# Optimization experiments

Hardware: AMD Instinct MI355X
Metric: run time of the kernel (lower is better)

## Reference

```python
import jax, jax.numpy as jnp
import numpy as np

INPUT_SIZE = 128
HIDDEN_SIZE = 256
OUTPUT_SIZE = 64
BATCH = 128
SEQ_LEN = 2048


def _xavier(key, shape):
    fan_in, fan_out = shape[1], shape[0]
    std = (2.0 / (fan_in + fan_out)) ** 0.5
    return jax.random.normal(key, shape, dtype=jnp.float32) * std


def setup_inputs() -> dict:
    key = jax.random.key(0)
    ks = jax.random.split(key, 5)
    gru_in = INPUT_SIZE + OUTPUT_SIZE  # Jordan feedback: input concat prev output
    return {
        "x": jax.random.normal(ks[0], (BATCH, SEQ_LEN, INPUT_SIZE), dtype=jnp.float32),
        "w_ih": _xavier(ks[1], (3 * HIDDEN_SIZE, gru_in)),   # [r|z|n] input weights
        "w_hh": _xavier(ks[2], (3 * HIDDEN_SIZE, HIDDEN_SIZE)),
        "b_ih": jnp.zeros((3 * HIDDEN_SIZE,), dtype=jnp.float32),
        "b_hh": jnp.zeros((3 * HIDDEN_SIZE,), dtype=jnp.float32),
        "fc_w": _xavier(ks[3], (OUTPUT_SIZE, HIDDEN_SIZE)),
        "fc_b": jnp.zeros((OUTPUT_SIZE,), dtype=jnp.float32),
    }


def reference(x, w_ih, w_hh, b_ih, b_hh, fc_w, fc_b):
    B = x.shape[0]
    H = w_hh.shape[1]
    O = fc_w.shape[0]

    def step(carry, x_t):
        h, y_prev = carry  # h: [B,H], y_prev: [B,O]
        inp = jnp.concatenate([x_t, y_prev], axis=-1)       # [B, I+O]
        gi = inp @ w_ih.T + b_ih                            # [B, 3H]
        gh = h @ w_hh.T + b_hh                              # [B, 3H]
        i_r, i_z, i_n = jnp.split(gi, 3, axis=-1)
        h_r, h_z, h_n = jnp.split(gh, 3, axis=-1)
        r = jax.nn.sigmoid(i_r + h_r)
        z = jax.nn.sigmoid(i_z + h_z)
        n = jnp.tanh(i_n + r * h_n)
        h_new = (1.0 - z) * n + z * h                       # PyTorch GRU update
        y = jnp.tanh(h_new @ fc_w.T + fc_b)                 # Jordan output feedback
        return (h_new, y), None

    xs = jnp.swapaxes(x, 0, 1)  # [T, B, I] for scan over time
    h0 = jnp.zeros((B, H), dtype=x.dtype)
    y0 = jnp.zeros((B, O), dtype=x.dtype)
    (h_last, y_last), _ = jax.lax.scan(step, (h0, y0), xs)
    return y_last  # matches outputs[:, -1, :]
```

## Files before the change

kernel.cpp:

```cpp
#include <hip/hip_runtime.h>
#include <math.h>


#define TSTEPS 2048
#define ISZ 128

typedef _Float16 half8 __attribute__((ext_vector_type(8)));
typedef float f32x4 __attribute__((ext_vector_type(4)));
typedef unsigned int u32;
typedef unsigned int u32x4 __attribute__((ext_vector_type(4)));
typedef unsigned long long u64;

__device__ __forceinline__ f32x4 mfma16(half8 a, half8 b, f32x4 c) {
  return __builtin_amdgcn_mfma_f32_16x16x32_f16(a, b, c, 0, 0, 0);
}
__device__ __forceinline__ float sigm(float x) {
  return __builtin_amdgcn_rcpf(1.f + __expf(-x));
}
__device__ __forceinline__ float tanh_fast(float x) {
  return 1.f - 2.f * __builtin_amdgcn_rcpf(1.f + __expf(2.f * x));
}
__device__ __forceinline__ float asf(u32 u) {
  union { u32 v; float f; } c; c.v = u; return c.f;
}

__device__ __forceinline__ void st_pkt(void* p, u32x4 v) {
  asm volatile("global_store_dwordx4 %0, %1, off sc1" :: "v"(p), "v"(v) : "memory");
}
__device__ __forceinline__ void ld_pkt3_issue(const void* p1, const void* p2,
                                              const void* p3, u32x4& r1, u32x4& r2,
                                              u32x4& r3) {
  asm volatile("global_load_dwordx4 %0, %3, off sc1\n\t"
               "global_load_dwordx4 %1, %4, off sc1\n\t"
               "global_load_dwordx4 %2, %5, off sc1"
               : "=&v"(r1), "=&v"(r2), "=&v"(r3)
               : "v"(p1), "v"(p2), "v"(p3) : "memory");
}
__device__ __forceinline__ void ld_pkt3_wait(const void* p1, const void* p2,
                                             const void* p3, u32x4& r1, u32x4& r2,
                                             u32x4& r3) {
  asm volatile("global_load_dwordx4 %0, %3, off sc1\n\t"
               "global_load_dwordx4 %1, %4, off sc1\n\t"
               "global_load_dwordx4 %2, %5, off sc1\n\t"
               "s_waitcnt vmcnt(0)"
               : "=&v"(r1), "=&v"(r2), "=&v"(r3)
               : "v"(p1), "v"(p2), "v"(p3) : "memory");
}
__device__ __forceinline__ void ld_x2(const float* p, u32x4& x0, u32x4& x1) {
  asm volatile("global_load_dwordx4 %0, %2, off\n\t"
               "global_load_dwordx4 %1, %3, off"
               : "=&v"(x0), "=&v"(x1)
               : "v"(p), "v"(p + 4) : "memory");
}
#define PKT_OK(r, tgt) (((r)[2] >= (tgt)) && (((r)[0] ^ (r)[1] ^ (r)[2]) == (r)[3]))
#define SB() __builtin_amdgcn_sched_barrier(0)

__global__ __attribute__((amdgpu_flat_work_group_size(256, 256),
                          amdgpu_waves_per_eu(1, 1)))
void jordan_rnn(const float* __restrict__ xg, const float* __restrict__ w_ih,
                const float* __restrict__ w_hh, const float* __restrict__ b_ih,
                const float* __restrict__ b_hh, const float* __restrict__ fc_w,
                const float* __restrict__ fc_b, float* __restrict__ out,
                unsigned char* __restrict__ ws)
{
  const int tid  = threadIdx.x;
  const int lane = tid & 63;
  const int wv   = tid >> 6;
  const int n    = lane & 15;
  const int quad = lane >> 4;
  const int col  = blockIdx.x & 7;
  const int q    = blockIdx.x >> 3;
  const int u0   = q * 64 + wv * 16;
  const int b0   = col * 16;

  unsigned char* pay = ws;

  __shared__ _Float16 act[16][456];
  {
    unsigned int* za = (unsigned int*)&act[0][0];
    for (int i = tid; i < 3648; i += 256) za[i] = 0u;
  }

  half8 wr[14], wz[14], win[6], whn[8], wfc[8];
  {
    const int kq = quad * 8;
    const int ur = u0 + n, uz = 256 + u0 + n, un = 512 + u0 + n;
#pragma unroll
    for (int kk = 0; kk < 6; ++kk) {
      const float* pr = w_ih + ur * 192 + kk * 32 + kq;
      const float* pz = w_ih + uz * 192 + kk * 32 + kq;
      const float* pn = w_ih + un * 192 + kk * 32 + kq;
#pragma unroll
      for (int j = 0; j < 8; ++j) {
        wr[kk][j] = (_Float16)pr[j]; wz[kk][j] = (_Float16)pz[j]; win[kk][j] = (_Float16)pn[j];
      }
    }
#pragma unroll
    for (int kk = 0; kk < 8; ++kk) {
      const float* pr = w_hh + ur * 256 + kk * 32 + kq;
      const float* pz = w_hh + uz * 256 + kk * 32 + kq;
      const float* pn = w_hh + un * 256 + kk * 32 + kq;
#pragma unroll
      for (int j = 0; j < 8; ++j) {
        wr[6 + kk][j] = (_Float16)pr[j]; wz[6 + kk][j] = (_Float16)pz[j]; whn[kk][j] = (_Float16)pn[j];
      }
    }
#pragma unroll
    for (int kk = 0; kk < 8; ++kk) {
      const float* pf = fc_w + (wv * 16 + n) * 256 + kk * 32 + kq;
#pragma unroll
      for (int j = 0; j < 8; ++j) wfc[kk][j] = (_Float16)pf[j];
    }
  }
  const float br   = b_ih[u0 + n] + b_hh[u0 + n];
  const float bz   = b_ih[256 + u0 + n] + b_hh[256 + u0 + n];
  const float bin_ = b_ih[512 + u0 + n];
  const float bhn  = b_hh[512 + u0 + n];
  const float fcb  = fc_b[wv * 16 + n];

  float hprev[4] = {0.f, 0.f, 0.f, 0.f};

  const int xr = tid >> 4, xc = tid & 15;
  const int sblk = tid >> 6, srem = tid & 63;
  const int cr = (srem >> 4) * 4;
  const int cc = srem & 15;
  const int ok0 = 6 + 2 * q;
  const int fk0 = 2 * q;
  const int q1 = (q + 1) & 3, q2 = (q + 2) & 3, q3 = (q + 3) & 3;

  unsigned char* cb0 = pay + (size_t)col * 16384;
  unsigned char* cb1 = cb0 + 131072;
  const int poff = (q * 4 + wv) * 1024 + lane * 16;
  const int off1 = (q1 * 4 + sblk) * 1024 + srem * 16;
  const int off2 = (q2 * 4 + sblk) * 1024 + srem * 16;
  const int off3 = (q3 * 4 + sblk) * 1024 + srem * 16;

  const float* xbase = xg + (size_t)(b0 + xr) * TSTEPS * ISZ + xc * 8;
  u32x4 xw0, xw1;

  {
    float4 a = *(const float4*)xbase, b = *(const float4*)(xbase + 4);
    union { _Float16 h[8]; uint4 u; } pk;
    pk.h[0]=(_Float16)a.x; pk.h[1]=(_Float16)a.y; pk.h[2]=(_Float16)a.z; pk.h[3]=(_Float16)a.w;
    pk.h[4]=(_Float16)b.x; pk.h[5]=(_Float16)b.y; pk.h[6]=(_Float16)b.z; pk.h[7]=(_Float16)b.w;
    *(uint4*)&act[xr][xc * 8] = pk.u;
    ld_x2(xbase + ISZ, xw0, xw1);
  }
  __syncthreads();

  for (int t = 1; t <= TSTEPS; ++t) {
    const u32 tgt = (u32)(t - 1);
    unsigned char* cb = ((t - 1) & 1) ? cb1 : cb0;

    u32x4 a1, a2, a3, b1, b2, b3, c1, c2, c3;
    ld_pkt3_issue(cb + off1, cb + off2, cb + off3, a1, a2, a3);

    f32x4 aR = {0,0,0,0}, aZ = {0,0,0,0}, aIN = {0,0,0,0}, aHN = {0,0,0,0};
    f32x4 accy = {0,0,0,0};
#pragma unroll
    for (int kk = 0; kk < 4; ++kk) {
      half8 af = *(const half8*)&act[n][kk * 32 + quad * 8];
      aR = mfma16(af, wr[kk], aR);
      aZ = mfma16(af, wz[kk], aZ);
      aIN = mfma16(af, win[kk], aIN);
    }
    ld_pkt3_issue(cb + off1, cb + off2, cb + off3, b1, b2, b3);

#pragma unroll
    for (int kk = 0; kk < 2; ++kk) {
      half8 af = *(const half8*)&act[n][(ok0 + kk) * 32 + quad * 8];
      aR = mfma16(af, wr[ok0 + kk], aR);
      aZ = mfma16(af, wz[ok0 + kk], aZ);
      aHN = mfma16(af, whn[ok0 - 6 + kk], aHN);
    }
    ld_pkt3_issue(cb + off1, cb + off2, cb + off3, c1, c2, c3);

#pragma unroll
    for (int kk = 0; kk < 2; ++kk) {
      half8 af = *(const half8*)&act[n][192 + (fk0 + kk) * 32 + quad * 8];
      accy = mfma16(af, wfc[fk0 + kk], accy);
    }

    u32x4 r1, r2, r3;
    SB();
    asm volatile("s_waitcnt vmcnt(6)" : "+v"(a1), "+v"(a2), "+v"(a3) :: "memory");
    SB();
    int ok = PKT_OK(a1, tgt) && PKT_OK(a2, tgt) && PKT_OK(a3, tgt);
    if (__all(ok)) {
      r1 = a1; r2 = a2; r3 = a3;
    } else {
      SB();
      asm volatile("s_waitcnt vmcnt(3)" : "+v"(b1), "+v"(b2), "+v"(b3) :: "memory");
      SB();
      ok = PKT_OK(b1, tgt) && PKT_OK(b2, tgt) && PKT_OK(b3, tgt);
      if (__all(ok)) {
        r1 = b1; r2 = b2; r3 = b3;
      } else {
        SB();
        asm volatile("s_waitcnt vmcnt(0)" : "+v"(c1), "+v"(c2), "+v"(c3) :: "memory");
        SB();
        r1 = c1; r2 = c2; r3 = c3;
        ok = PKT_OK(r1, tgt) && PKT_OK(r2, tgt) && PKT_OK(r3, tgt);
        while (!__all(ok)) {
          __builtin_amdgcn_s_sleep(1);
          ld_pkt3_wait(cb + off1, cb + off2, cb + off3, r1, r2, r3);
          ok = PKT_OK(r1, tgt) && PKT_OK(r2, tgt) && PKT_OK(r3, tgt);
        }
      }
    }
    {
      union { u64 u; _Float16 h[4]; } w1, w2, w3;
      w1.u = ((u64)r1[1] << 32) | r1[0];
      w2.u = ((u64)r2[1] << 32) | r2[0];
      w3.u = ((u64)r3[1] << 32) | r3[0];
#pragma unroll
      for (int r = 0; r < 4; ++r) {
        act[cr + r][192 + q1 * 64 + sblk * 16 + cc] = w1.h[r];
        act[cr + r][192 + q2 * 64 + sblk * 16 + cc] = w2.h[r];
        act[cr + r][192 + q3 * 64 + sblk * 16 + cc] = w3.h[r];
      }
    }
    __syncthreads();

#pragma unroll
    for (int kk = 6; kk < 14; ++kk) {
      if (kk == ok0 || kk == ok0 + 1) continue;
      half8 af = *(const half8*)&act[n][kk * 32 + quad * 8];
      aR = mfma16(af, wr[kk], aR);
      aZ = mfma16(af, wz[kk], aZ);
      aHN = mfma16(af, whn[kk - 6], aHN);
    }
#pragma unroll
    for (int kk = 0; kk < 8; ++kk) {
      if (kk == fk0 || kk == fk0 + 1) continue;
      half8 af = *(const half8*)&act[n][192 + kk * 32 + quad * 8];
      accy = mfma16(af, wfc[kk], accy);
    }
    if (t > 1) {
#pragma unroll
      for (int r = 0; r < 4; ++r)
        act[quad * 4 + r][128 + wv * 16 + n] = (_Float16)tanh_fast(accy[r] + fcb);
    }
    {
      union { _Float16 h[8]; uint4 u; } pk;
      pk.h[0]=(_Float16)asf(xw0[0]); pk.h[1]=(_Float16)asf(xw0[1]);
      pk.h[2]=(_Float16)asf(xw0[2]); pk.h[3]=(_Float16)asf(xw0[3]);
      pk.h[4]=(_Float16)asf(xw1[0]); pk.h[5]=(_Float16)asf(xw1[1]);
      pk.h[6]=(_Float16)asf(xw1[2]); pk.h[7]=(_Float16)asf(xw1[3]);
      *(uint4*)&act[xr][xc * 8] = pk.u;
      const size_t ts = (t + 1 < TSTEPS) ? (size_t)(t + 1) : (size_t)(TSTEPS - 1);
      ld_x2(xbase + ts * ISZ, xw0, xw1);
    }
    __syncthreads();

#pragma unroll
    for (int kk = 4; kk < 6; ++kk) {
      half8 af = *(const half8*)&act[n][kk * 32 + quad * 8];
      aR = mfma16(af, wr[kk], aR);
      aZ = mfma16(af, wz[kk], aZ);
      aIN = mfma16(af, win[kk], aIN);
    }
    {
      union { _Float16 h[4]; u64 u; } ph;
#pragma unroll
      for (int r = 0; r < 4; ++r) {
        float rg = sigm(aR[r] + br);
        float zg = sigm(aZ[r] + bz);
        float nn = tanh_fast(aIN[r] + bin_ + rg * (aHN[r] + bhn));
        float hv = (1.f - zg) * nn + zg * hprev[r];
        hprev[r] = hv;
        ph.h[r] = (_Float16)hv;
      }
      unsigned char* cbw = (t & 1) ? cb1 : cb0;
      u32x4 pkt;
      pkt[0] = (u32)ph.u; pkt[1] = (u32)(ph.u >> 32); pkt[2] = (u32)t;
      pkt[3] = pkt[0] ^ pkt[1] ^ pkt[2];
      st_pkt(cbw + poff, pkt);
#pragma unroll
      for (int r = 0; r < 4; ++r)
        act[quad * 4 + r][192 + u0 + n] = ph.h[r];
    }
    __syncthreads();
  }

  if (q == 0) {
    const u32 tgt = (u32)TSTEPS;
    unsigned char* cb = (TSTEPS & 1) ? cb1 : cb0;

    u32x4 r1, r2, r3;
    ld_pkt3_issue(cb + off1, cb + off2, cb + off3, r1, r2, r3);

    f32x4 accy = {0,0,0,0};
#pragma unroll
    for (int kk = 0; kk < 2; ++kk) {
      half8 af = *(const half8*)&act[n][192 + (fk0 + kk) * 32 + quad * 8];
      accy = mfma16(af, wfc[fk0 + kk], accy);
    }

    SB();
    asm volatile("s_waitcnt vmcnt(0)" : "+v"(r1), "+v"(r2), "+v"(r3) :: "memory");
    SB();
    {
      int ok = PKT_OK(r1, tgt) && PKT_OK(r2, tgt) && PKT_OK(r3, tgt);
      while (!__all(ok)) {
        __builtin_amdgcn_s_sleep(1);
        ld_pkt3_wait(cb + off1, cb + off2, cb + off3, r1, r2, r3);
        ok = PKT_OK(r1, tgt) && PKT_OK(r2, tgt) && PKT_OK(r3, tgt);
      }
    }
    {
      union { u64 u; _Float16 h[4]; } w1, w2, w3;
      w1.u = ((u64)r1[1] << 32) | r1[0];
      w2.u = ((u64)r2[1] << 32) | r2[0];
      w3.u = ((u64)r3[1] << 32) | r3[0];
#pragma unroll
      for (int r = 0; r < 4; ++r) {
        act[cr + r][192 + q1 * 64 + sblk * 16 + cc] = w1.h[r];
        act[cr + r][192 + q2 * 64 + sblk * 16 + cc] = w2.h[r];
        act[cr + r][192 + q3 * 64 + sblk * 16 + cc] = w3.h[r];
      }
    }
    __syncthreads();

#pragma unroll
    for (int kk = 0; kk < 8; ++kk) {
      if (kk == fk0 || kk == fk0 + 1) continue;
      half8 af = *(const half8*)&act[n][192 + kk * 32 + quad * 8];
      accy = mfma16(af, wfc[kk], accy);
    }
#pragma unroll
    for (int r = 0; r < 4; ++r)
      out[(size_t)(b0 + quad * 4 + r) * 64 + wv * 16 + n] = tanh_fast(accy[r] + fcb);
  }
}

extern "C" void kernel_launch(void* const* d_in, const int* in_sizes, int n_in,
                              void* d_out, int out_size, void* d_ws, size_t ws_size,
                              hipStream_t stream) {
  hipMemsetAsync(d_ws, 0, 262144, stream);
  jordan_rnn<<<dim3(32), dim3(256), 0, stream>>>(
      (const float*)d_in[0], (const float*)d_in[1], (const float*)d_in[2],
      (const float*)d_in[3], (const float*)d_in[4], (const float*)d_in[5],
      (const float*)d_in[6], (float*)d_out, (unsigned char*)d_ws);
}
```

Before: 4.797 ms.

## Process two batch columns per block, halving grid and interleaving their recurrences

Each workgroup now handles two 16-row batch tiles (A and B) instead of one, launching 16 blocks instead of 32. The two independent recurrences are interleaved so the MFMA work of one can overlap the cross-block packet polling latency of the other, and the weight registers are reused across both tiles. The cost is that each block does twice the serial MFMA and elementwise work per step. The speculative three-stage packet polling is also replaced with a single wait per tile.

Result: slower. 7.503 ms (+56.4%).

```diff
diff --git a/kernel.cpp b/kernel.cpp
--- a/kernel.cpp
+++ b/kernel.cpp
@@ -68,17 +68,18 @@
   const int wv   = tid >> 6;
   const int n    = lane & 15;
   const int quad = lane >> 4;
-  const int col  = blockIdx.x & 7;
-  const int q    = blockIdx.x >> 3;
+  const int pr   = blockIdx.x & 3;
+  const int q    = blockIdx.x >> 2;
+  const int colA = pr * 2, colB = pr * 2 + 1;
   const int u0   = q * 64 + wv * 16;
-  const int b0   = col * 16;
+  const int b0A  = colA * 16, b0B = colB * 16;
 
   unsigned char* pay = ws;
 
-  __shared__ _Float16 act[16][456];
+  __shared__ _Float16 act[2][16][456];
   {
-    unsigned int* za = (unsigned int*)&act[0][0];
-    for (int i = tid; i < 3648; i += 256) za[i] = 0u;
+    u32* za = (u32*)&act[0][0][0];
+    for (int i = tid; i < 7296; i += 256) za[i] = 0u;
   }
 
   half8 wr[14], wz[14], win[6], whn[8], wfc[8];
@@ -87,22 +88,22 @@
     const int ur = u0 + n, uz = 256 + u0 + n, un = 512 + u0 + n;
 #pragma unroll
     for (int kk = 0; kk < 6; ++kk) {
-      const float* pr = w_ih + ur * 192 + kk * 32 + kq;
+      const float* prr = w_ih + ur * 192 + kk * 32 + kq;
       const float* pz = w_ih + uz * 192 + kk * 32 + kq;
       const float* pn = w_ih + un * 192 + kk * 32 + kq;
 #pragma unroll
       for (int j = 0; j < 8; ++j) {
-        wr[kk][j] = (_Float16)pr[j]; wz[kk][j] = (_Float16)pz[j]; win[kk][j] = (_Float16)pn[j];
-      }
-    }
-#pragma unroll
-    for (int kk = 0; kk < 8; ++kk) {
-      const float* pr = w_hh + ur * 256 + kk * 32 + kq;
+        wr[kk][j] = (_Float16)prr[j]; wz[kk][j] = (_Float16)pz[j]; win[kk][j] = (_Float16)pn[j];
+      }
+    }
+#pragma unroll
+    for (int kk = 0; kk < 8; ++kk) {
+      const float* prr = w_hh + ur * 256 + kk * 32 + kq;
       const float* pz = w_hh + uz * 256 + kk * 32 + kq;
       const float* pn = w_hh + un * 256 + kk * 32 + kq;
 #pragma unroll
       for (int j = 0; j < 8; ++j) {
-        wr[6 + kk][j] = (_Float16)pr[j]; wz[6 + kk][j] = (_Float16)pz[j]; whn[kk][j] = (_Float16)pn[j];
+        wr[6 + kk][j] = (_Float16)prr[j]; wz[6 + kk][j] = (_Float16)pz[j]; whn[kk][j] = (_Float16)pn[j];
       }
     }
 #pragma unroll
@@ -118,7 +119,8 @@
   const float bhn  = b_hh[512 + u0 + n];
   const float fcb  = fc_b[wv * 16 + n];
 
-  float hprev[4] = {0.f, 0.f, 0.f, 0.f};
+  float hpA[4] = {0.f, 0.f, 0.f, 0.f};
+  float hpB[4] = {0.f, 0.f, 0.f, 0.f};
 
   const int xr = tid >> 4, xc = tid & 15;
   const int sblk = tid >> 6, srem = tid & 63;
@@ -128,96 +130,122 @@
   const int fk0 = 2 * q;
   const int q1 = (q + 1) & 3, q2 = (q + 2) & 3, q3 = (q + 3) & 3;
 
-  unsigned char* cb0 = pay + (size_t)col * 16384;
-  unsigned char* cb1 = cb0 + 131072;
+  unsigned char* cbA0 = pay + (size_t)colA * 16384;
+  unsigned char* cbA1 = cbA0 + 131072;
+  unsigned char* cbB0 = pay + (size_t)colB * 16384;
+  unsigned char* cbB1 = cbB0 + 131072;
   const int poff = (q * 4 + wv) * 1024 + lane * 16;
   const int off1 = (q1 * 4 + sblk) * 1024 + srem * 16;
   const int off2 = (q2 * 4 + sblk) * 1024 + srem * 16;
   const int off3 = (q3 * 4 + sblk) * 1024 + srem * 16;
 
-  const float* xbase = xg + (size_t)(b0 + xr) * TSTEPS * ISZ + xc * 8;
-  u32x4 xw0, xw1;
+  const float* xbA = xg + (size_t)(b0A + xr) * TSTEPS * ISZ + xc * 8;
+  const float* xbB = xg + (size_t)(b0B + xr) * TSTEPS * ISZ + xc * 8;
+  u32x4 xwA0, xwA1, xwB0, xwB1;
 
   {
-    float4 a = *(const float4*)xbase, b = *(const float4*)(xbase + 4);
+    float4 a = *(const float4*)xbA, b = *(const float4*)(xbA + 4);
     union { _Float16 h[8]; uint4 u; } pk;
     pk.h[0]=(_Float16)a.x; pk.h[1]=(_Float16)a.y; pk.h[2]=(_Float16)a.z; pk.h[3]=(_Float16)a.w;
     pk.h[4]=(_Float16)b.x; pk.h[5]=(_Float16)b.y; pk.h[6]=(_Float16)b.z; pk.h[7]=(_Float16)b.w;
-    *(uint4*)&act[xr][xc * 8] = pk.u;
-    ld_x2(xbase + ISZ, xw0, xw1);
+    *(uint4*)&act[0][xr][xc * 8] = pk.u;
+    float4 c = *(const float4*)xbB, d = *(const float4*)(xbB + 4);
+    pk.h[0]=(_Float16)c.x; pk.h[1]=(_Float16)c.y; pk.h[2]=(_Float16)c.z; pk.h[3]=(_Float16)c.w;
+    pk.h[4]=(_Float16)d.x; pk.h[5]=(_Float16)d.y; pk.h[6]=(_Float16)d.z; pk.h[7]=(_Float16)d.w;
+    *(uint4*)&act[1][xr][xc * 8] = pk.u;
+    ld_x2(xbA + ISZ, xwA0, xwA1);
+    ld_x2(xbB + ISZ, xwB0, xwB1);
   }
   __syncthreads();
 
   for (int t = 1; t <= TSTEPS; ++t) {
     const u32 tgt = (u32)(t - 1);
-    unsigned char* cb = ((t - 1) & 1) ? cb1 : cb0;
-
-    u32x4 a1, a2, a3, b1, b2, b3, c1, c2, c3;
-    ld_pkt3_issue(cb + off1, cb + off2, cb + off3, a1, a2, a3);
-
-    f32x4 aR = {0,0,0,0}, aZ = {0,0,0,0}, aIN = {0,0,0,0}, aHN = {0,0,0,0};
-    f32x4 accy = {0,0,0,0};
+    unsigned char* cbA = ((t - 1) & 1) ? cbA1 : cbA0;
+    unsigned char* cbB = ((t - 1) & 1) ? cbB1 : cbB0;
+
+    u32x4 a1, a2, a3, b1, b2, b3;
+    ld_pkt3_issue(cbA + off1, cbA + off2, cbA + off3, a1, a2, a3);
+    ld_pkt3_issue(cbB + off1, cbB + off2, cbB + off3, b1, b2, b3);
+
+    f32x4 RA = {0,0,0,0}, ZA = {0,0,0,0}, NA = {0,0,0,0}, HA = {0,0,0,0}, YA = {0,0,0,0};
+    f32x4 RB = {0,0,0,0}, ZB = {0,0,0,0}, NB = {0,0,0,0}, HB = {0,0,0,0}, YB = {0,0,0,0};
 #pragma unroll
     for (int kk = 0; kk < 4; ++kk) {
-      half8 af = *(const half8*)&act[n][kk * 32 + quad * 8];
-      aR = mfma16(af, wr[kk], aR);
-      aZ = mfma16(af, wz[kk], aZ);
-      aIN = mfma16(af, win[kk], aIN);
-    }
-    ld_pkt3_issue(cb + off1, cb + off2, cb + off3, b1, b2, b3);
-
-#pragma unroll
-    for (int kk = 0; kk < 2; ++kk) {
-      half8 af = *(const half8*)&act[n][(ok0 + kk) * 32 + quad * 8];
-      aR = mfma16(af, wr[ok0 + kk], aR);
-      aZ = mfma16(af, wz[ok0 + kk], aZ);
-      aHN = mfma16(af, whn[ok0 - 6 + kk], aHN);
-    }
-    ld_pkt3_issue(cb + off1, cb + off2, cb + off3, c1, c2, c3);
-
-#pragma unroll
-    for (int kk = 0; kk < 2; ++kk) {
-      half8 af = *(const half8*)&act[n][192 + (fk0 + kk) * 32 + quad * 8];
-      accy = mfma16(af, wfc[fk0 + kk], accy);
-    }
-
-    u32x4 r1, r2, r3;
-    SB();
-    asm volatile("s_waitcnt vmcnt(6)" : "+v"(a1), "+v"(a2), "+v"(a3) :: "memory");
-    SB();
-    int ok = PKT_OK(a1, tgt) && PKT_OK(a2, tgt) && PKT_OK(a3, tgt);
-    if (__all(ok)) {
-      r1 = a1; r2 = a2; r3 = a3;
-    } else {
-      SB();
-      asm volatile("s_waitcnt vmcnt(3)" : "+v"(b1), "+v"(b2), "+v"(b3) :: "memory");
-      SB();
-      ok = PKT_OK(b1, tgt) && PKT_OK(b2, tgt) && PKT_OK(b3, tgt);
-      if (__all(ok)) {
-        r1 = b1; r2 = b2; r3 = b3;
-      } else {
-        SB();
-        asm volatile("s_waitcnt vmcnt(0)" : "+v"(c1), "+v"(c2), "+v"(c3) :: "memory");
-        SB();
-        r1 = c1; r2 = c2; r3 = c3;
-        ok = PKT_OK(r1, tgt) && PKT_OK(r2, tgt) && PKT_OK(r3, tgt);
-        while (!__all(ok)) {
-          __builtin_amdgcn_s_sleep(1);
-          ld_pkt3_wait(cb + off1, cb + off2, cb + off3, r1, r2, r3);
-          ok = PKT_OK(r1, tgt) && PKT_OK(r2, tgt) && PKT_OK(r3, tgt);
-        }
+      half8 af = *(const half8*)&act[0][n][kk * 32 + quad * 8];
+      RA = mfma16(af, wr[kk], RA); ZA = mfma16(af, wz[kk], ZA); NA = mfma16(af, win[kk], NA);
+    }
+#pragma unroll
+    for (int kk = 0; kk < 2; ++kk) {
+      half8 af = *(const half8*)&act[0][n][(ok0 + kk) * 32 + quad * 8];
+      RA = mfma16(af, wr[ok0 + kk], RA); ZA = mfma16(af, wz[ok0 + kk], ZA);
+      HA = mfma16(af, whn[ok0 - 6 + kk], HA);
+    }
+#pragma unroll
+    for (int kk = 0; kk < 2; ++kk) {
+      half8 af = *(const half8*)&act[0][n][192 + (fk0 + kk) * 32 + quad * 8];
+      YA = mfma16(af, wfc[fk0 + kk], YA);
+    }
+#pragma unroll
+    for (int kk = 0; kk < 4; ++kk) {
+      half8 af = *(const half8*)&act[1][n][kk * 32 + quad * 8];
+      RB = mfma16(af, wr[kk], RB); ZB = mfma16(af, wz[kk], ZB); NB = mfma16(af, win[kk], NB);
+    }
+#pragma unroll
+    for (int kk = 0; kk < 2; ++kk) {
+      half8 af = *(const half8*)&act[1][n][(ok0 + kk) * 32 + quad * 8];
+      RB = mfma16(af, wr[ok0 + kk], RB); ZB = mfma16(af, wz[ok0 + kk], ZB);
+      HB = mfma16(af, whn[ok0 - 6 + kk], HB);
+    }
+#pragma unroll
+    for (int kk = 0; kk < 2; ++kk) {
+      half8 af = *(const half8*)&act[1][n][192 + (fk0 + kk) * 32 + quad * 8];
+      YB = mfma16(af, wfc[fk0 + kk], YB);
+    }
+
+    SB();
+    asm volatile("s_waitcnt vmcnt(3)" : "+v"(a1), "+v"(a2), "+v"(a3) :: "memory");
+    SB();
+    {
+      int ok = PKT_OK(a1, tgt) && PKT_OK(a2, tgt) && PKT_OK(a3, tgt);
+      while (!__all(ok)) {
+        __builtin_amdgcn_s_sleep(1);
+        ld_pkt3_wait(cbA + off1, cbA + off2, cbA + off3, a1, a2, a3);
+        ok = PKT_OK(a1, tgt) && PKT_OK(a2, tgt) && PKT_OK(a3, tgt);
       }
     }
     {
       union { u64 u; _Float16 h[4]; } w1, w2, w3;
-      w1.u = ((u64)r1[1] << 32) | r1[0];
-      w2.u = ((u64)r2[1] << 32) | r2[0];
-      w3.u = ((u64)r3[1] << 32) | r3[0];
-#pragma unroll
-      for (int r = 0; r < 4; ++r) {
-        act[cr + r][192 + q1 * 64 + sblk * 16 + cc] = w1.h[r];
-        act[cr + r][192 + q2 * 64 + sblk * 16 + cc] = w2.h[r];
-        act[cr + r][192 + q3 * 64 + sblk * 16 + cc] = w3.h[r];
+      w1.u = ((u64)a1[1] << 32) | a1[0];
+      w2.u = ((u64)a2[1] << 32) | a2[0];
+      w3.u = ((u64)a3[1] << 32) | a3[0];
+#pragma unroll
+      for (int r = 0; r < 4; ++r) {
+        act[0][cr + r][192 + q1 * 64 + sblk * 16 + cc] = w1.h[r];
+        act[0][cr + r][192 + q2 * 64 + sblk * 16 + cc] = w2.h[r];
+        act[0][cr + r][192 + q3 * 64 + sblk * 16 + cc] = w3.h[r];
+      }
+    }
+    SB();
+    asm volatile("s_waitcnt vmcnt(0)" : "+v"(b1), "+v"(b2), "+v"(b3) :: "memory");
+    SB();
+    {
+      int ok = PKT_OK(b1, tgt) && PKT_OK(b2, tgt) && PKT_OK(b3, tgt);
+      while (!__all(ok)) {
+        __builtin_amdgcn_s_sleep(1);
+        ld_pkt3_wait(cbB + off1, cbB + off2, cbB + off3, b1, b2, b3);
+        ok = PKT_OK(b1, tgt) && PKT_OK(b2, tgt) && PKT_OK(b3, tgt);
+      }
+    }
+    {
+      union { u64 u; _Float16 h[4]; } w1, w2, w3;
+      w1.u = ((u64)b1[1] << 32) | b1[0];
+      w2.u = ((u64)b2[1] << 32) | b2[0];
+      w3.u = ((u64)b3[1] << 32) | b3[0];
+#pragma unroll
+      for (int r = 0; r < 4; ++r) {
+        act[1][cr + r][192 + q1 * 64 + sblk * 16 + cc] = w1.h[r];
+        act[1][cr + r][192 + q2 * 64 + sblk * 16 + cc] = w2.h[r];
+        act[1][cr + r][192 + q3 * 64 + sblk * 16 + cc] = w3.h[r];
       }
     }
     __syncthreads();
@@ -225,99 +253,179 @@
 #pragma unroll
     for (int kk = 6; kk < 14; ++kk) {
       if (kk == ok0 || kk == ok0 + 1) continue;
-      half8 af = *(const half8*)&act[n][kk * 32 + quad * 8];
-      aR = mfma16(af, wr[kk], aR);
-      aZ = mfma16(af, wz[kk], aZ);
-      aHN = mfma16(af, whn[kk - 6], aHN);
+      half8 af = *(const half8*)&act[0][n][kk * 32 + quad * 8];
+      RA = mfma16(af, wr[kk], RA); ZA = mfma16(af, wz[kk], ZA);
+      HA = mfma16(af, whn[kk - 6], HA);
     }
 #pragma unroll
     for (int kk = 0; kk < 8; ++kk) {
       if (kk == fk0 || kk == fk0 + 1) continue;
-      half8 af = *(const half8*)&act[n][192 + kk * 32 + quad * 8];
-      accy = mfma16(af, wfc[kk], accy);
+      half8 af = *(const half8*)&act[0][n][192 + kk * 32 + quad * 8];
+      YA = mfma16(af, wfc[kk], YA);
     }
     if (t > 1) {
 #pragma unroll
       for (int r = 0; r < 4; ++r)
-        act[quad * 4 + r][128 + wv * 16 + n] = (_Float16)tanh_fast(accy[r] + fcb);
+        act[0][quad * 4 + r][128 + wv * 16 + n] = (_Float16)tanh_fast(YA[r] + fcb);
     }
     {
       union { _Float16 h[8]; uint4 u; } pk;
-      pk.h[0]=(_Float16)asf(xw0[0]); pk.h[1]=(_Float16)asf(xw0[1]);
-      pk.h[2]=(_Float16)asf(xw0[2]); pk.h[3]=(_Float16)asf(xw0[3]);
-      pk.h[4]=(_Float16)asf(xw1[0]); pk.h[5]=(_Float16)asf(xw1[1]);
-      pk.h[6]=(_Float16)asf(xw1[2]); pk.h[7]=(_Float16)asf(xw1[3]);
-      *(uint4*)&act[xr][xc * 8] = pk.u;
+      pk.h[0]=(_Float16)asf(xwA0[0]); pk.h[1]=(_Float16)asf(xwA0[1]);
+      pk.h[2]=(_Float16)asf(xwA0[2]); pk.h[3]=(_Float16)asf(xwA0[3]);
+      pk.h[4]=(_Float16)asf(xwA1[0]); pk.h[5]=(_Float16)asf(xwA1[1]);
+      pk.h[6]=(_Float16)asf(xwA1[2]); pk.h[7]=(_Float16)asf(xwA1[3]);
+      *(uint4*)&act[0][xr][xc * 8] = pk.u;
       const size_t ts = (t + 1 < TSTEPS) ? (size_t)(t + 1) : (size_t)(TSTEPS - 1);
-      ld_x2(xbase + ts * ISZ, xw0, xw1);
+      ld_x2(xbA + ts * ISZ, xwA0, xwA1);
+    }
+#pragma unroll
+    for (int kk = 6; kk < 14; ++kk) {
+      if (kk == ok0 || kk == ok0 + 1) continue;
+      half8 af = *(const half8*)&act[1][n][kk * 32 + quad * 8];
+      RB = mfma16(af, wr[kk], RB); ZB = mfma16(af, wz[kk], ZB);
+      HB = mfma16(af, whn[kk - 6], HB);
+    }
+#pragma unroll
+    for (int kk = 0; kk < 8; ++kk) {
+      if (kk == fk0 || kk == fk0 + 1) continue;
+      half8 af = *(const half8*)&act[1][n][192 + kk * 32 + quad * 8];
+      YB = mfma16(af, wfc[kk], YB);
+    }
+    if (t > 1) {
+#pragma unroll
+      for (int r = 0; r < 4; ++r)
+        act[1][quad * 4 + r][128 + wv * 16 + n] = (_Float16)tanh_fast(YB[r] + fcb);
+    }
+    {
+      union { _Float16 h[8]; uint4 u; } pk;
+      pk.h[0]=(_Float16)asf(xwB0[0]); pk.h[1]=(_Float16)asf(xwB0[1]);
+      pk.h[2]=(_Float16)asf(xwB0[2]); pk.h[3]=(_Float16)asf(xwB0[3]);
+      pk.h[4]=(_Float16)asf(xwB1[0]); pk.h[5]=(_Float16)asf(xwB1[1]);
+      pk.h[6]=(_Float16)asf(xwB1[2]); pk.h[7]=(_Float16)asf(xwB1[3]);
+      *(uint4*)&act[1][xr][xc * 8] = pk.u;
+      const size_t ts = (t + 1 < TSTEPS) ? (size_t)(t + 1) : (size_t)(TSTEPS - 1);
+      ld_x2(xbB + ts * ISZ, xwB0, xwB1);
     }
     __syncthreads();
 
 #pragma unroll
     for (int kk = 4; kk < 6; ++kk) {
-      half8 af = *(const half8*)&act[n][kk * 32 + quad * 8];
-      aR = mfma16(af, wr[kk], aR);
-      aZ = mfma16(af, wz[kk], aZ);
-      aIN = mfma16(af, win[kk], aIN);
+      half8 af = *(const half8*)&act[0][n][kk * 32 + quad * 8];
+      RA = mfma16(af, wr[kk], RA); ZA = mfma16(af, wz[kk], ZA); NA = mfma16(af, win[kk], NA);
     }
     {
       union { _Float16 h[4]; u64 u; } ph;
 #pragma unroll
       for (int r = 0; r < 4; ++r) {
-        float rg = sigm(aR[r] + br);
-        float zg = sigm(aZ[r] + bz);
-        float nn = tanh_fast(aIN[r] + bin_ + rg * (aHN[r] + bhn));
-        float hv = (1.f - zg) * nn + zg * hprev[r];
-        hprev[r] = hv;
+        float rg = sigm(RA[r] + br);
+        float zg = sigm(ZA[r] + bz);
+        float nn = tanh_fast(NA[r] + bin_ + rg * (HA[r] + bhn));
+        float hv = (1.f - zg) * nn + zg * hpA[r];
+        hpA[r] = hv;
         ph.h[r] = (_Float16)hv;
       }
-      unsigned char* cbw = (t & 1) ? cb1 : cb0;
+      unsigned char* cbw = (t & 1) ? cbA1 : cbA0;
       u32x4 pkt;
       pkt[0] = (u32)ph.u; pkt[1] = (u32)(ph.u >> 32); pkt[2] = (u32)t;
       pkt[3] = pkt[0] ^ pkt[1] ^ pkt[2];
       st_pkt(cbw + poff, pkt);
 #pragma unroll
       for (int r = 0; r < 4; ++r)
-        act[quad * 4 + r][192 + u0 + n] = ph.h[r];
+        act[0][quad * 4 + r][192 + u0 + n] = ph.h[r];
+    }
+#pragma unroll
+    for (int kk = 4; kk < 6; ++kk) {
+      half8 af = *(const half8*)&act[1][n][kk * 32 + quad * 8];
+      RB = mfma16(af, wr[kk], RB); ZB = mfma16(af, wz[kk], ZB); NB = mfma16(af, win[kk], NB);
+    }
+    {
+      union { _Float16 h[4]; u64 u; } ph;
+#pragma unroll
+      for (int r = 0; r < 4; ++r) {
+        float rg = sigm(RB[r] + br);
+        float zg = sigm(ZB[r] + bz);
+        float nn = tanh_fast(NB[r] + bin_ + rg * (HB[r] + bhn));
+        float hv = (1.f - zg) * nn + zg * hpB[r];
+        hpB[r] = hv;
+        ph.h[r] = (_Float16)hv;
+      }
+      unsigned char* cbw = (t & 1) ? cbB1 : cbB0;
+      u32x4 pkt;
+      pkt[0] = (u32)ph.u; pkt[1] = (u32)(ph.u >> 32); pkt[2] = (u32)t;
+      pkt[3] = pkt[0] ^ pkt[1] ^ pkt[2];
+      st_pkt(cbw + poff, pkt);
+#pragma unroll
+      for (int r = 0; r < 4; ++r)
+        act[1][quad * 4 + r][192 + u0 + n] = ph.h[r];
     }
     __syncthreads();
   }
 
   if (q == 0) {
     const u32 tgt = (u32)TSTEPS;
-    unsigned char* cb = (TSTEPS & 1) ? cb1 : cb0;
-
-    u32x4 r1, r2, r3;
-    ld_pkt3_issue(cb + off1, cb + off2, cb + off3, r1, r2, r3);
-
-    f32x4 accy = {0,0,0,0};
-#pragma unroll
-    for (int kk = 0; kk < 2; ++kk) {
-      half8 af = *(const half8*)&act[n][192 + (fk0 + kk) * 32 + quad * 8];
-      accy = mfma16(af, wfc[fk0 + kk], accy);
-    }
-
-    SB();
-    asm volatile("s_waitcnt vmcnt(0)" : "+v"(r1), "+v"(r2), "+v"(r3) :: "memory");
-    SB();
-    {
-      int ok = PKT_OK(r1, tgt) && PKT_OK(r2, tgt) && PKT_OK(r3, tgt);
+    unsigned char* cbA = (TSTEPS & 1) ? cbA1 : cbA0;
+    unsigned char* cbB = (TSTEPS & 1) ? cbB1 : cbB0;
+
+    u32x4 a1, a2, a3, b1, b2, b3;
+    ld_pkt3_issue(cbA + off1, cbA + off2, cbA + off3, a1, a2, a3);
+    ld_pkt3_issue(cbB + off1, cbB + off2, cbB + off3, b1, b2, b3);
+
+    f32x4 YA = {0,0,0,0}, YB = {0,0,0,0};
+#pragma unroll
+    for (int kk = 0; kk < 2; ++kk) {
+      half8 af = *(const half8*)&act[0][n][192 + (fk0 + kk) * 32 + quad * 8];
+      YA = mfma16(af, wfc[fk0 + kk], YA);
+    }
+#pragma unroll
+    for (int kk = 0; kk < 2; ++kk) {
+      half8 af = *(const half8*)&act[1][n][192 + (fk0 + kk) * 32 + quad * 8];
+      YB = mfma16(af, wfc[fk0 + kk], YB);
+    }
+
+    SB();
+    asm volatile("s_waitcnt vmcnt(3)" : "+v"(a1), "+v"(a2), "+v"(a3) :: "memory");
+    SB();
+    {
+      int ok = PKT_OK(a1, tgt) && PKT_OK(a2, tgt) && PKT_OK(a3, tgt);
       while (!__all(ok)) {
         __builtin_amdgcn_s_sleep(1);
-        ld_pkt3_wait(cb + off1, cb + off2, cb + off3, r1, r2, r3);
-        ok = PKT_OK(r1, tgt) && PKT_OK(r2, tgt) && PKT_OK(r3, tgt);
+        ld_pkt3_wait(cbA + off1, cbA + off2, cbA + off3, a1, a2, a3);
+        ok = PKT_OK(a1, tgt) && PKT_OK(a2, tgt) && PKT_OK(a3, tgt);
       }
     }
     {
       union { u64 u; _Float16 h[4]; } w1, w2, w3;
-      w1.u = ((u64)r1[1] << 32) | r1[0];
-      w2.u = ((u64)r2[1] << 32) | r2[0];
-      w3.u = ((u64)r3[1] << 32) | r3[0];
-#pragma unroll
-      for (int r = 0; r < 4; ++r) {
-        act[cr + r][192 + q1 * 64 + sblk * 16 + cc] = w1.h[r];
-        act[cr + r][192 + q2 * 64 + sblk * 16 + cc] = w2.h[r];
-        act[cr + r][192 + q3 * 64 + sblk * 16 + cc] = w3.h[r];
+      w1.u = ((u64)a1[1] << 32) | a1[0];
+      w2.u = ((u64)a2[1] << 32) | a2[0];
+      w3.u = ((u64)a3[1] << 32) | a3[0];
+#pragma unroll
+      for (int r = 0; r < 4; ++r) {
+        act[0][cr + r][192 + q1 * 64 + sblk * 16 + cc] = w1.h[r];
+        act[0][cr + r][192 + q2 * 64 + sblk * 16 + cc] = w2.h[r];
+        act[0][cr + r][192 + q3 * 64 + sblk * 16 + cc] = w3.h[r];
+      }
+    }
+    SB();
+    asm volatile("s_waitcnt vmcnt(0)" : "+v"(b1), "+v"(b2), "+v"(b3) :: "memory");
+    SB();
+    {
+      int ok = PKT_OK(b1, tgt) && PKT_OK(b2, tgt) && PKT_OK(b3, tgt);
+      while (!__all(ok)) {
+        __builtin_amdgcn_s_sleep(1);
+        ld_pkt3_wait(cbB + off1, cbB + off2, cbB + off3, b1, b2, b3);
+        ok = PKT_OK(b1, tgt) && PKT_OK(b2, tgt) && PKT_OK(b3, tgt);
+      }
+    }
+    {
+      union { u64 u; _Float16 h[4]; } w1, w2, w3;
+      w1.u = ((u64)b1[1] << 32) | b1[0];
+      w2.u = ((u64)b2[1] << 32) | b2[0];
+      w3.u = ((u64)b3[1] << 32) | b3[0];
+#pragma unroll
+      for (int r = 0; r < 4; ++r) {
+        act[1][cr + r][192 + q1 * 64 + sblk * 16 + cc] = w1.h[r];
+        act[1][cr + r][192 + q2 * 64 + sblk * 16 + cc] = w2.h[r];
+        act[1][cr + r][192 + q3 * 64 + sblk * 16 + cc] = w3.h[r];
       }
     }
     __syncthreads();
@@ -325,12 +433,20 @@
 #pragma unroll
     for (int kk = 0; kk < 8; ++kk) {
       if (kk == fk0 || kk == fk0 + 1) continue;
-      half8 af = *(const half8*)&act[n][192 + kk * 32 + quad * 8];
-      accy = mfma16(af, wfc[kk], accy);
-    }
-#pragma unroll
-    for (int r = 0; r < 4; ++r)
-      out[(size_t)(b0 + quad * 4 + r) * 64 + wv * 16 + n] = tanh_fast(accy[r] + fcb);
+      half8 af = *(const half8*)&act[0][n][192 + kk * 32 + quad * 8];
+      YA = mfma16(af, wfc[kk], YA);
+    }
+#pragma unroll
+    for (int kk = 0; kk < 8; ++kk) {
+      if (kk == fk0 || kk == fk0 + 1) continue;
+      half8 af = *(const half8*)&act[1][n][192 + kk * 32 + quad * 8];
+      YB = mfma16(af, wfc[kk], YB);
+    }
+#pragma unroll
+    for (int r = 0; r < 4; ++r) {
+      out[(size_t)(b0A + quad * 4 + r) * 64 + wv * 16 + n] = tanh_fast(YA[r] + fcb);
+      out[(size_t)(b0B + quad * 4 + r) * 64 + wv * 16 + n] = tanh_fast(YB[r] + fcb);
+    }
   }
 }
 
@@ -338,7 +454,7 @@
                               void* d_out, int out_size, void* d_ws, size_t ws_size,
                               hipStream_t stream) {
   hipMemsetAsync(d_ws, 0, 262144, stream);
-  jordan_rnn<<<dim3(32), dim3(256), 0, stream>>>(
+  jordan_rnn<<<dim3(16), dim3(256), 0, stream>>>(
       (const float*)d_in[0], (const float*)d_in[1], (const float*)d_in[2],
       (const float*)d_in[3], (const float*)d_in[4], (const float*)d_in[5],
       (const float*)d_in[6], (float*)d_out, (unsigned char*)d_ws);
```
